# Kernel tuning notes

Hardware: AMD Instinct MI355X
Metric: run time of the kernel (lower is better)

Reference implementation:

```python
import jax, jax.numpy as jnp
import numpy as np
from jax import lax

TAU = 2.0        # LIFNode default tau, decay_input=True, v_reset=0.0
V_TH = 1.0       # default threshold
SG_ALPHA = 4.0   # surrogate.Sigmoid default alpha
EPS = 1e-5


@jax.custom_vjp
def spike_fn(v):
    return (v >= V_TH).astype(v.dtype)

def _spike_fwd(v):
    return spike_fn(v), v

def _spike_bwd(v, g):
    sg = jax.nn.sigmoid(SG_ALPHA * (v - V_TH))
    return (g * SG_ALPHA * sg * (1.0 - sg),)

spike_fn.defvjp(_spike_fwd, _spike_bwd)


def lif(x_seq):
    """Multi-step LIF: x_seq [T, ...] -> spikes [T, ...]. Hard reset to 0."""
    def step(v, x):
        v = v + (x - v) / TAU          # decay_input integration, v_reset=0
        s = spike_fn(v)
        v = v * (1.0 - s)              # hard reset
        return v, s
    v0 = jnp.zeros_like(x_seq[0])
    _, s_seq = lax.scan(step, v0, x_seq)
    return s_seq


def conv3x3(x, w):
    # x [N,C,H,W], w [O,I,3,3], padding=1, no bias
    return lax.conv_general_dilated(x, w, (1, 1), ((1, 1), (1, 1)),
                                    dimension_numbers=('NCHW', 'OIHW', 'NCHW'))


def tdbn(x, gamma, beta):
    # ThresholdDependentBatchNorm2d: BN over merged (T*B, H, W) per channel
    m = x.mean(axis=(0, 2, 3), keepdims=True)
    v = x.var(axis=(0, 2, 3), keepdims=True)
    return (x - m) * lax.rsqrt(v + EPS) * gamma[None, :, None, None] + beta[None, :, None, None]


def maxpool2(x):
    return lax.reduce_window(x, -jnp.inf, lax.max, (1, 1, 2, 2), (1, 1, 2, 2), 'VALID')


def setup_inputs() -> dict:
    key = jax.random.key(0)
    ks = jax.random.split(key, 5)
    T, B, H, W = 16, 32, 32, 400
    x = jax.random.normal(ks[0], (T, B, 1, H, W), dtype=jnp.float32)
    w1 = jax.random.normal(ks[1], (6, 1, 3, 3), dtype=jnp.float32) * (1.0 / 3.0)
    w2 = jax.random.normal(ks[2], (6, 6, 3, 3), dtype=jnp.float32) * (1.0 / jnp.sqrt(54.0))
    w3 = jax.random.normal(ks[3], (6, 6, 3, 3), dtype=jnp.float32) * (1.0 / jnp.sqrt(54.0))
    kf = jax.random.split(ks[4], 2)
    fw1 = jax.random.normal(kf[0], (100, 1200), dtype=jnp.float32) * (1.0 / jnp.sqrt(1200.0))
    fw2 = jax.random.normal(kf[1], (2, 100), dtype=jnp.float32) * (1.0 / 10.0)
    ones6 = jnp.ones((6,), jnp.float32)
    zeros6 = jnp.zeros((6,), jnp.float32)
    return {"x": x, "w1": w1, "g1": ones6, "b1": zeros6,
            "w2": w2, "g2": ones6, "b2": zeros6,
            "w3": w3, "g3": ones6, "b3": zeros6,
            "fw1": fw1, "fw2": fw2}


def _forward(x, w1, g1, b1, w2, g2, b2, w3, g3, b3, fw1, fw2):
    T, B = x.shape[0], x.shape[1]

    def block(s_seq, w, g, b):
        # conv + tdBN + LIF + maxpool over [T,B,C,H,W]
        TB = s_seq.reshape((T * B,) + s_seq.shape[2:])
        y = tdbn(conv3x3(TB, w), g, b)
        y = y.reshape((T, B) + y.shape[1:])
        s = lif(y)
        p = maxpool2(s.reshape((T * B,) + s.shape[2:]))
        return p.reshape((T, B) + p.shape[1:])

    h = block(x, w1, g1, b1)
    h = block(h, w2, g2, b2)
    h = block(h, w3, g3, b3)          # [T, B, 6, 4, 50]

    h = h.reshape(T, B, -1)            # flatten (C,H,W) -> 1200
    h = lif(jnp.einsum('tbf,of->tbo', h, fw1))   # [T, B, 100]
    out = lif(jnp.einsum('tbf,of->tbo', h, fw2)) # [T, B, 2]
    return out


def reference(x, w1, g1, b1, w2, g2, b2, w3, g3, b3, fw1, fw2):
    return _forward(x, w1, g1, b1, w2, g2, b2, w3, g3, b3, fw1, fw2)
```

## Files before the change

kernel.cpp:

```cpp
#include <hip/hip_runtime.h>


namespace {

constexpr int T = 16, B = 32;
constexpr int H1 = 32, W1 = 400, P1H = 16, P1W = 200;
constexpr int H2 = 16, W2 = 200, P2H = 8,  P2W = 100;
constexpr int H3 = 8,  W3 = 100, P3H = 4,  P3W = 50;

constexpr int NWG_S1 = T * B * (H1 / 32) * (W1 / 100);
constexpr int NWG_F1 = B * (P1H / 4) * (P1W / 10);
constexpr int NWG_F2 = B * (P2H / 4) * (P2W / 5);

constexpr size_t OFF_PART1  = 0;
constexpr size_t OFF_PARTF1 = OFF_PART1 + (size_t)NWG_S1 * 12 * 8;
constexpr size_t OFF_PARTF2 = OFF_PARTF1 + (size_t)6400 * 12 * 8;
constexpr size_t OFF_STATS  = OFF_PARTF2 + (size_t)2560 * 12 * 8;
constexpr size_t OFF_POOL1  = 1310720;
constexpr size_t OFF_POOL2  = OFF_POOL1 + (size_t)T * B * 6 * P1H * P1W * 4;
constexpr size_t OFF_POOL3  = OFF_POOL2 + (size_t)T * B * 6 * P2H * P2W * 4;
constexpr size_t OFF_U1     = OFF_POOL3 + (size_t)T * B * 6 * P3H * P3W * 4;

}

#define LDS_PHASE_BARRIER()                                   \
  do {                                                        \
    asm volatile("s_waitcnt lgkmcnt(0)" ::: "memory");        \
    __builtin_amdgcn_s_barrier();                             \
    __builtin_amdgcn_sched_barrier(0);                        \
  } while (0)

__device__ __forceinline__ float lif_step(float& v, float y) {
  v = v + (y - v) * 0.5f;
  float sp = (v >= 1.0f) ? 1.0f : 0.0f;
  v = (sp > 0.0f) ? 0.0f : v;
  return sp;
}

__device__ __forceinline__ void reduce12(double* s, double* q, double* partials) {
  __shared__ double lds[4][12];
  int lane = threadIdx.x & 63, wid = threadIdx.x >> 6;
#pragma unroll
  for (int k = 0; k < 12; k++) {
    double v = (k < 6) ? s[k] : q[k - 6];
#pragma unroll
    for (int off = 32; off >= 1; off >>= 1) v += __shfl_down(v, off, 64);
    if (lane == 0) lds[wid][k] = v;
  }
  __syncthreads();
  if (threadIdx.x < 12) {
    partials[(size_t)blockIdx.x * 12 + threadIdx.x] =
        lds[0][threadIdx.x] + lds[1][threadIdx.x] + lds[2][threadIdx.x] + lds[3][threadIdx.x];
  }
}

__device__ __forceinline__ void reduce12_sel(int oidx, double s_acc, double q_acc,
                                             double* partials) {
  __shared__ double lds[4][12];
  int lane = threadIdx.x & 63, wid = threadIdx.x >> 6;
#pragma unroll
  for (int k = 0; k < 12; k++) {
    double v = (k == oidx) ? s_acc : ((k == oidx + 6) ? q_acc : 0.0);
#pragma unroll
    for (int off = 32; off >= 1; off >>= 1) v += __shfl_down(v, off, 64);
    if (lane == 0) lds[wid][k] = v;
  }
  __syncthreads();
  if (threadIdx.x < 12) {
    partials[(size_t)blockIdx.x * 12 + threadIdx.x] =
        lds[0][threadIdx.x] + lds[1][threadIdx.x] + lds[2][threadIdx.x] + lds[3][threadIdx.x];
  }
}

template <int NC, int H, int W, int TH, int TW>
__global__ void conv_stats_lds(const float* __restrict__ in, const float* __restrict__ wt,
                               double* __restrict__ partials) {
  constexpr int IH = TH + 2, IW = TW + 2;
  constexpr int IWP = (IW & 1) ? IW : IW + 1;
  constexpr int NW = NC * 54;
  constexpr int NTH = H / TH, NTW = W / TW;
  constexpr int NT = NTH * NTW;
  __shared__ float wsm[NW];
  __shared__ float tile[NC][IH][IWP];

  int tid = threadIdx.x;
  for (int k = tid; k < NW; k += blockDim.x) wsm[k] = wt[k];

  int wg = blockIdx.x;
  int tb = wg / NT;
  int ti = wg % NT;
  int ty = ti / NTW, tx = ti % NTW;
  int h0 = ty * TH - 1, w0 = tx * TW - 1;
  const float* xb = in + (size_t)tb * NC * H * W;

  for (int k = tid; k < NC * IH * IW; k += blockDim.x) {
    int i = k / (IH * IW);
    int r = k % (IH * IW);
    int rr = r / IW, cc = r % IW;
    int hh = h0 + rr, ww = w0 + cc;
    tile[i][rr][cc] = (hh >= 0 && hh < H && ww >= 0 && ww < W) ? xb[i * H * W + hh * W + ww] : 0.0f;
  }
  __syncthreads();

  double s[6] = {0, 0, 0, 0, 0, 0}, q[6] = {0, 0, 0, 0, 0, 0};
  for (int pos = tid; pos < TH * TW; pos += blockDim.x) {
    int ly = pos / TW, lx = pos % TW;
    float acc[6] = {0, 0, 0, 0, 0, 0};
#pragma unroll
    for (int i = 0; i < NC; i++) {
      float p[9];
#pragma unroll
      for (int ky = 0; ky < 3; ky++)
#pragma unroll
        for (int kx = 0; kx < 3; kx++) p[ky * 3 + kx] = tile[i][ly + ky][lx + kx];
#pragma unroll
      for (int o = 0; o < 6; o++) {
        float a = acc[o];
#pragma unroll
        for (int k2 = 0; k2 < 9; k2++) a = fmaf(p[k2], wsm[(o * NC + i) * 9 + k2], a);
        acc[o] = a;
      }
    }
#pragma unroll
    for (int o = 0; o < 6; o++) {
      s[o] += (double)acc[o];
      q[o] += (double)acc[o] * (double)acc[o];
    }
  }
  reduce12(s, q, partials);
}

__global__ void finalize_stats(const double* __restrict__ partials, int nb, double n,
                               const float* __restrict__ gamma,
                               float* __restrict__ mean_out, float* __restrict__ sg_out) {
  __shared__ double red0[256];
  __shared__ double red1[256];
  int ch = blockIdx.x;
  int tid = threadIdx.x;
  double a0 = 0.0, a1 = 0.0;
  for (int b = tid; b < nb; b += 256) {
    a0 += partials[(size_t)b * 12 + ch];
    a1 += partials[(size_t)b * 12 + ch + 6];
  }
  red0[tid] = a0;
  red1[tid] = a1;
  __syncthreads();
#pragma unroll
  for (int off = 128; off >= 1; off >>= 1) {
    if (tid < off) {
      red0[tid] += red0[tid + off];
      red1[tid] += red1[tid + off];
    }
    __syncthreads();
  }
  if (tid == 0) {
    double mean = red0[0] / n;
    double var = red1[0] / n - mean * mean;
    double invstd = 1.0 / sqrt(var + 1e-5);
    mean_out[ch] = (float)mean;
    sg_out[ch] = (float)(invstd * (double)gamma[ch]);
  }
}

__global__ void fuse1_stats(const float* __restrict__ x, const float* __restrict__ w1g,
                            const float* __restrict__ w2g,
                            const float* __restrict__ mean1, const float* __restrict__ sg1,
                            const float* __restrict__ beta1,
                            float* __restrict__ pool1, double* __restrict__ partials2) {
  __shared__ float wsm1[54];
  __shared__ float wsm2[324];
  __shared__ float til[2][14][13];
  __shared__ float phl[432];
  __shared__ float pr[40][7][7];

  int tid = threadIdx.x;
  for (int k = tid; k < 54; k += 256) wsm1[k] = w1g[k];
  for (int k = tid; k < 324; k += 256) wsm2[k] = w2g[k];

  int wg = blockIdx.x;
  int b = wg / 80;
  int rem = wg % 80;
  int oy = rem / 20, ox = rem % 20;
  int iy0 = 8 * oy - 3, ix0 = 20 * ox - 3;

  bool s_in[2];
  int s_off[2], s_lofs[2];
#pragma unroll
  for (int j = 0; j < 2; j++) {
    int k = tid + 256 * j;
    bool valid = k < 364;
    int srr = k / 26, scc = k % 26;
    int shh = iy0 + srr, sww = ix0 + scc;
    s_in[j] = valid && shh >= 0 && shh < H1 && sww >= 0 && sww < W1;
    s_off[j] = shh * W1 + sww;
    s_lofs[j] = valid ? ((scc & 1) * 182 + srr * 13 + (scc >> 1)) : -1;
  }
  float* tilf = &til[0][0][0];

  int hch[2], hhy[2], hhx[2], hpy[2], hpx[2];
  bool hact[2], hval[2], hown[2];
  float m_[2], sc_[2], be_[2];
  float wv[2][9];
#pragma unroll
  for (int sl = 0; sl < 2; sl++) {
    int pos = tid + 256 * sl;
    hact[sl] = pos < 432;
    int p2 = hact[sl] ? pos : 0;
    int ch = p2 / 72;
    int r = p2 % 72;
    int hy = r / 12, hx = r % 12;
    hch[sl] = ch; hhy[sl] = hy; hhx[sl] = hx;
    int py = 4 * oy - 1 + hy, px = 10 * ox - 1 + hx;
    hpy[sl] = py; hpx[sl] = px;
    hval[sl] = hact[sl] && py >= 0 && py < P1H && px >= 0 && px < P1W;
    hown[sl] = hact[sl] && hy >= 1 && hy <= 4 && hx >= 1 && hx <= 10;
#pragma unroll
    for (int k = 0; k < 9; k++) wv[sl][k] = w1g[ch * 9 + k];
    m_[sl] = mean1[ch]; sc_[sl] = sg1[ch]; be_[sl] = beta1[ch];
  }

  int oidx = (tid < 240) ? (tid / 40) : -1;
  int pos40 = tid % 40;
  int psy = pos40 / 10, psx = pos40 % 10;

  float v[2][4];
#pragma unroll
  for (int sl = 0; sl < 2; sl++)
#pragma unroll
    for (int k = 0; k < 4; k++) v[sl][k] = 0.0f;
  double s_acc = 0.0, q_acc = 0.0;

  float rs[2] = {0.0f, 0.0f};
#pragma unroll
  for (int j = 0; j < 2; j++)
    if (s_in[j]) rs[j] = x[(size_t)(0 * B + b) * (H1 * W1) + s_off[j]];

  for (int t = 0; t < T; t++) {
    __syncthreads();
#pragma unroll
    for (int j = 0; j < 2; j++)
      if (s_lofs[j] >= 0) tilf[s_lofs[j]] = rs[j];
    if (t + 1 < T) {
#pragma unroll
      for (int j = 0; j < 2; j++)
        if (s_in[j]) rs[j] = x[(size_t)((t + 1) * B + b) * (H1 * W1) + s_off[j]];
    }
    LDS_PHASE_BARRIER();
#pragma unroll
    for (int sl = 0; sl < 2; sl++) {
      if (hact[sl]) {
        float smax = 0.0f;
        if (hval[sl]) {
          int ry = 2 * hhy[sl], hx = hhx[sl];
          float p[16];
#pragma unroll
          for (int r = 0; r < 4; r++) {
            p[r * 4 + 0] = til[0][ry + r][hx];
            p[r * 4 + 1] = til[1][ry + r][hx];
            p[r * 4 + 2] = til[0][ry + r][hx + 1];
            p[r * 4 + 3] = til[1][ry + r][hx + 1];
          }
#pragma unroll
          for (int dy = 0; dy < 2; dy++) {
#pragma unroll
            for (int dx = 0; dx < 2; dx++) {
              float acc = 0.0f;
#pragma unroll
              for (int ky = 0; ky < 3; ky++)
#pragma unroll
                for (int kx = 0; kx < 3; kx++)
                  acc = fmaf(p[(dy + ky) * 4 + dx + kx], wv[sl][ky * 3 + kx], acc);
              float y = (acc - m_[sl]) * sc_[sl] + be_[sl];
              float sp = lif_step(v[sl][dy * 2 + dx], y);
              smax = fmaxf(smax, sp);
            }
          }
        }
        phl[tid + 256 * sl] = smax;
        if (hown[sl])
          pool1[((size_t)(t * B + b) * 6 + hch[sl]) * (P1H * P1W) + hpy[sl] * P1W + hpx[sl]] = smax;
      }
    }
    LDS_PHASE_BARRIER();
    if (oidx >= 0) {
      int i2 = oidx;
      float pt[9];
#pragma unroll
      for (int ky = 0; ky < 3; ky++)
#pragma unroll
        for (int kx = 0; kx < 3; kx++)
          pt[ky * 3 + kx] = phl[i2 * 72 + (psy + ky) * 12 + (psx + kx)];
      float p6[6];
#pragma unroll
      for (int o = 0; o < 6; o++) {
        float a = 0.0f;
#pragma unroll
        for (int k2 = 0; k2 < 9; k2++) a = fmaf(pt[k2], wsm2[(o * 6 + i2) * 9 + k2], a);
        p6[o] = a;
      }
#pragma unroll
      for (int o = 0; o < 6; o++) pr[pos40][i2][o] = p6[o];
    }
    LDS_PHASE_BARRIER();
    if (oidx >= 0) {
      double acc = 0.0;
#pragma unroll
      for (int ic = 0; ic < 6; ic++) acc += (double)pr[pos40][ic][oidx];
      s_acc += acc;
      q_acc += acc * acc;
    }
  }
  __syncthreads();
  reduce12_sel(oidx, s_acc, q_acc, partials2);
}

__global__ void fuse2_stats(const float* __restrict__ in, const float* __restrict__ w2g,
                            const float* __restrict__ w3g,
                            const float* __restrict__ mean2, const float* __restrict__ sg2,
                            const float* __restrict__ beta2,
                            float* __restrict__ pool2, double* __restrict__ partials3) {
  __shared__ float wsm2[324];
  __shared__ float wsm3[324];
  __shared__ float til[2][6][14][9];
  __shared__ float phl[6][6][7];
  __shared__ float pr[20][6][7];

  int tid = threadIdx.x;
  for (int k = tid; k < 324; k += 256) { wsm2[k] = w2g[k]; wsm3[k] = w3g[k]; }

  int wg = blockIdx.x;
  int b = wg / 40;
  int rem = wg % 40;
  int oy = rem / 20, ox = rem % 20;
  int iy0 = 8 * oy - 3, ix0 = 10 * ox - 3;
  constexpr int HW = H2 * W2;

  bool s_in[6];
  int s_off[6], s_lofs[6];
#pragma unroll
  for (int j = 0; j < 6; j++) {
    int k = tid + 256 * j;
    bool valid = k < 1344;
    int i = k / 224;
    int r2 = k % 224;
    int rr = r2 / 16, cc = r2 % 16;
    int hh = iy0 + rr, ww = ix0 + cc;
    s_in[j] = valid && hh >= 0 && hh < H2 && ww >= 0 && ww < W2;
    s_off[j] = i * HW + hh * W2 + ww;
    s_lofs[j] = valid ? ((cc & 1) * 756 + i * 126 + rr * 9 + (cc >> 1)) : -1;
  }
  float* tilf = &til[0][0][0][0];

  bool active = tid < 252;
  int ch = 0, hy = 0, hx = 0, py = 0, px = 0;
  bool pvalid = false, own = false;
  if (active) {
    ch = tid / 42;
    int r = tid % 42;
    hy = r / 7; hx = r % 7;
    py = 4 * oy - 1 + hy; px = 5 * ox - 1 + hx;
    pvalid = (py >= 0 && py < P2H && px >= 0 && px < P2W);
    own = (hy >= 1 && hy <= 4 && hx >= 1 && hx <= 5);
  }
  float m = active ? mean2[ch] : 0.0f;
  float sc = active ? sg2[ch] : 0.0f;
  float be = active ? beta2[ch] : 0.0f;

  int oidx = (tid < 120) ? (tid / 20) : -1;
  int pos = tid % 20;
  int psy = pos / 5, psx = pos % 5;

  float v[4] = {0.0f, 0.0f, 0.0f, 0.0f};
  double s_acc = 0.0, q_acc = 0.0;

  float rs[6] = {0.0f, 0.0f, 0.0f, 0.0f, 0.0f, 0.0f};
  {
    const float* xb = in + (size_t)(0 * B + b) * 6 * HW;
#pragma unroll
    for (int j = 0; j < 6; j++)
      if (s_in[j]) rs[j] = xb[s_off[j]];
  }

  for (int t = 0; t < T; t++) {
    __syncthreads();
#pragma unroll
    for (int j = 0; j < 6; j++)
      if (s_lofs[j] >= 0) tilf[s_lofs[j]] = rs[j];
    if (t + 1 < T) {
      const float* xb = in + (size_t)((t + 1) * B + b) * 6 * HW;
#pragma unroll
      for (int j = 0; j < 6; j++)
        if (s_in[j]) rs[j] = xb[s_off[j]];
    }
    LDS_PHASE_BARRIER();
    if (active) {
      float smax = 0.0f;
      if (pvalid) {
        int ry = 2 * hy;
        float acc4[4] = {0.0f, 0.0f, 0.0f, 0.0f};
#pragma unroll
        for (int i = 0; i < 6; i++) {
          float p[16];
#pragma unroll
          for (int r = 0; r < 4; r++) {
            p[r * 4 + 0] = til[0][i][ry + r][hx];
            p[r * 4 + 1] = til[1][i][ry + r][hx];
            p[r * 4 + 2] = til[0][i][ry + r][hx + 1];
            p[r * 4 + 3] = til[1][i][ry + r][hx + 1];
          }
          const float* wo = &wsm2[(ch * 6 + i) * 9];
#pragma unroll
          for (int dy = 0; dy < 2; dy++)
#pragma unroll
            for (int dx = 0; dx < 2; dx++) {
              float a = acc4[dy * 2 + dx];
#pragma unroll
              for (int ky = 0; ky < 3; ky++)
#pragma unroll
                for (int kx = 0; kx < 3; kx++)
                  a = fmaf(p[(dy + ky) * 4 + dx + kx], wo[ky * 3 + kx], a);
              acc4[dy * 2 + dx] = a;
            }
        }
#pragma unroll
        for (int p4 = 0; p4 < 4; p4++) {
          float y = (acc4[p4] - m) * sc + be;
          float sp = lif_step(v[p4], y);
          smax = fmaxf(smax, sp);
        }
      }
      phl[ch][hy][hx] = smax;
      if (own)
        pool2[((size_t)(t * B + b) * 6 + ch) * (P2H * P2W) + py * P2W + px] = smax;
    }
    LDS_PHASE_BARRIER();
    if (oidx >= 0) {
      float pt[9];
#pragma unroll
      for (int ky = 0; ky < 3; ky++)
#pragma unroll
        for (int kx = 0; kx < 3; kx++)
          pt[ky * 3 + kx] = phl[oidx][psy + ky][psx + kx];
      float p6[6];
#pragma unroll
      for (int o = 0; o < 6; o++) {
        float a = 0.0f;
#pragma unroll
        for (int k2 = 0; k2 < 9; k2++) a = fmaf(pt[k2], wsm3[(o * 6 + oidx) * 9 + k2], a);
        p6[o] = a;
      }
#pragma unroll
      for (int o = 0; o < 6; o++) pr[pos][oidx][o] = p6[o];
    }
    LDS_PHASE_BARRIER();
    if (oidx >= 0) {
      double acc = 0.0;
#pragma unroll
      for (int ic = 0; ic < 6; ic++) acc += (double)pr[pos][ic][oidx];
      s_acc += acc;
      q_acc += acc * acc;
    }
  }
  __syncthreads();
  reduce12_sel(oidx, s_acc, q_acc, partials3);
}

template <int H, int W, int PH, int PW, int TH, int TW>
__global__ void block6_fuse_lds(const float* __restrict__ in, const float* __restrict__ wt,
                                const float* __restrict__ mean, const float* __restrict__ sg,
                                const float* __restrict__ beta, float* __restrict__ out) {
  constexpr int NTH = PH / TH, NTW = PW / TW;
  constexpr int IH = 2 * TH + 2, IW = 2 * TW + 2;
  constexpr int EW = IW / 2;
  constexpr int TILE_N = IH * IW;
  constexpr int NACT = 6 * TH * TW;
  constexpr int HW = H * W;
  __shared__ float wsm[324];
  __shared__ float til_e[6][IH][EW];
  __shared__ float til_o[6][IH][EW];

  for (int k = threadIdx.x; k < 324; k += blockDim.x) wsm[k] = wt[k];

  int wg = blockIdx.x;
  int b = wg / (NTH * NTW);
  int tid2 = wg % (NTH * NTW);
  int ty = tid2 / NTW, tx = tid2 % NTW;
  int h_in0 = 2 * (ty * TH) - 1, w_in0 = 2 * (tx * TW) - 1;

  int tid = threadIdx.x;
  int o = 0, lph = 0, lpw = 0;
  if (tid < NACT) {
    o = tid / (TH * TW);
    int r = tid % (TH * TW);
    lph = r / TW; lpw = r % TW;
  }
  float m = mean[o], s = sg[o], be = beta[o];
  float v[4] = {0.0f, 0.0f, 0.0f, 0.0f};

  for (int t = 0; t < T; t++) {
    __syncthreads();
    const float* xb = in + (size_t)(t * B + b) * 6 * HW;
    for (int k = tid; k < 6 * TILE_N; k += blockDim.x) {
      int i = k / TILE_N;
      int r2 = k % TILE_N;
      int rr = r2 / IW, cc = r2 % IW;
      int hh = h_in0 + rr, ww = w_in0 + cc;
      float val = (hh >= 0 && hh < H && ww >= 0 && ww < W) ? xb[i * HW + hh * W + ww] : 0.0f;
      if (cc & 1) til_o[i][rr][cc >> 1] = val;
      else        til_e[i][rr][cc >> 1] = val;
    }
    __syncthreads();
    if (tid < NACT) {
      int ry = 2 * lph;
      float acc[4] = {0.0f, 0.0f, 0.0f, 0.0f};
#pragma unroll
      for (int i = 0; i < 6; i++) {
        float p[16];
#pragma unroll
        for (int r = 0; r < 4; r++) {
          p[r * 4 + 0] = til_e[i][ry + r][lpw];
          p[r * 4 + 1] = til_o[i][ry + r][lpw];
          p[r * 4 + 2] = til_e[i][ry + r][lpw + 1];
          p[r * 4 + 3] = til_o[i][ry + r][lpw + 1];
        }
        const float* wo = &wsm[(o * 6 + i) * 9];
#pragma unroll
        for (int dy = 0; dy < 2; dy++)
#pragma unroll
          for (int dx = 0; dx < 2; dx++) {
            float a = acc[dy * 2 + dx];
#pragma unroll
            for (int ky = 0; ky < 3; ky++)
#pragma unroll
              for (int kx = 0; kx < 3; kx++)
                a = fmaf(p[(dy + ky) * 4 + dx + kx], wo[ky * 3 + kx], a);
            acc[dy * 2 + dx] = a;
          }
      }
      float smax = 0.0f;
#pragma unroll
      for (int p4 = 0; p4 < 4; p4++) {
        float y = (acc[p4] - m) * s + be;
        float sp = lif_step(v[p4], y);
        smax = fmaxf(smax, sp);
      }
      out[((size_t)(t * B + b) * 6 + o) * (PH * PW) + (ty * TH + lph) * PW + (tx * TW + lpw)] = smax;
    }
  }
}

__global__ void fc1_mm(const float* __restrict__ p3, const float* __restrict__ fw1,
                       float* __restrict__ u1) {
  int idx = blockIdx.x * blockDim.x + threadIdx.x;
  if (idx >= T * B * 100) return;
  int o = idx % 100;
  int tb = idx / 100;
  const float4* x4 = (const float4*)(p3 + (size_t)tb * 1200);
  const float4* w4 = (const float4*)(fw1 + (size_t)o * 1200);
  float acc = 0.0f;
#pragma unroll 4
  for (int k = 0; k < 300; k++) {
    float4 a = x4[k], w = w4[k];
    acc = fmaf(a.x, w.x, acc);
    acc = fmaf(a.y, w.y, acc);
    acc = fmaf(a.z, w.z, acc);
    acc = fmaf(a.w, w.w, acc);
  }
  u1[idx] = acc;
}

__global__ void fc_tail(const float* __restrict__ u1, const float* __restrict__ fw2,
                        float* __restrict__ outp) {
  __shared__ float s1[100];
  __shared__ float w2s[200];
  int b = blockIdx.x;
  int tid = threadIdx.x;
  for (int k = tid; k < 200; k += 128) w2s[k] = fw2[k];
  float v1 = 0.0f, v2 = 0.0f;
  __syncthreads();
  for (int t = 0; t < T; t++) {
    if (tid < 100) {
      float sp = lif_step(v1, u1[(size_t)(t * B + b) * 100 + tid]);
      s1[tid] = sp;
    }
    __syncthreads();
    if (tid < 2) {
      const float* wr = &w2s[tid * 100];
      float acc = 0.0f;
#pragma unroll
      for (int k = 0; k < 100; k++) acc = fmaf(s1[k], wr[k], acc);
      float sp = lif_step(v2, acc);
      outp[(size_t)(t * B + b) * 2 + tid] = sp;
    }
    __syncthreads();
  }
}

extern "C" void kernel_launch(void* const* d_in, const int* in_sizes, int n_in,
                              void* d_out, int out_size, void* d_ws, size_t ws_size,
                              hipStream_t stream) {
  const float* x   = (const float*)d_in[0];
  const float* w1  = (const float*)d_in[1];
  const float* g1  = (const float*)d_in[2];
  const float* b1  = (const float*)d_in[3];
  const float* w2  = (const float*)d_in[4];
  const float* g2  = (const float*)d_in[5];
  const float* b2  = (const float*)d_in[6];
  const float* w3  = (const float*)d_in[7];
  const float* g3  = (const float*)d_in[8];
  const float* b3  = (const float*)d_in[9];
  const float* fw1 = (const float*)d_in[10];
  const float* fw2 = (const float*)d_in[11];
  float* out = (float*)d_out;

  char* ws = (char*)d_ws;
  double* part1  = (double*)(ws + OFF_PART1);
  double* partf1 = (double*)(ws + OFF_PARTF1);
  double* partf2 = (double*)(ws + OFF_PARTF2);
  float* mean1 = (float*)(ws + OFF_STATS + 0);
  float* sg1   = (float*)(ws + OFF_STATS + 32);
  float* mean2 = (float*)(ws + OFF_STATS + 64);
  float* sg2   = (float*)(ws + OFF_STATS + 96);
  float* mean3 = (float*)(ws + OFF_STATS + 128);
  float* sg3   = (float*)(ws + OFF_STATS + 160);
  float* pool1 = (float*)(ws + OFF_POOL1);
  float* pool2 = (float*)(ws + OFF_POOL2);
  float* pool3 = (float*)(ws + OFF_POOL3);
  float* u1    = (float*)(ws + OFF_U1);

  conv_stats_lds<1, H1, W1, 32, 100><<<NWG_S1, 256, 0, stream>>>(x, w1, part1);
  finalize_stats<<<6, 256, 0, stream>>>(part1, NWG_S1, (double)T * B * H1 * W1, g1, mean1, sg1);
  fuse1_stats<<<NWG_F1, 256, 0, stream>>>(x, w1, w2, mean1, sg1, b1, pool1, partf1);
  finalize_stats<<<6, 256, 0, stream>>>(partf1, NWG_F1, (double)T * B * H2 * W2, g2, mean2, sg2);
  fuse2_stats<<<NWG_F2, 256, 0, stream>>>(pool1, w2, w3, mean2, sg2, b2, pool2, partf2);
  finalize_stats<<<6, 256, 0, stream>>>(partf2, NWG_F2, (double)T * B * H3 * W3, g3, mean3, sg3);
  {
    int nwg = B * (P3H / 2) * (P3W / 5);
    block6_fuse_lds<H3, W3, P3H, P3W, 2, 5><<<nwg, 64, 0, stream>>>(pool2, w3, mean3, sg3, b3, pool3);
  }
  {
    int n = T * B * 100;
    fc1_mm<<<(n + 255) / 256, 256, 0, stream>>>(pool3, fw1, u1);
  }
  fc_tail<<<B, 128, 0, stream>>>(u1, fw2, out);
}
```

Before: 368.7 us.

## Restructure FC1 as per-row workgroup with wave reductions; parallelize FC2 dot

```diff
diff --git a/kernel.cpp b/kernel.cpp
--- a/kernel.cpp
+++ b/kernel.cpp
@@ -551,22 +551,21 @@
 
 __global__ void fc1_mm(const float* __restrict__ p3, const float* __restrict__ fw1,
                        float* __restrict__ u1) {
-  int idx = blockIdx.x * blockDim.x + threadIdx.x;
-  if (idx >= T * B * 100) return;
-  int o = idx % 100;
-  int tb = idx / 100;
-  const float4* x4 = (const float4*)(p3 + (size_t)tb * 1200);
-  const float4* w4 = (const float4*)(fw1 + (size_t)o * 1200);
-  float acc = 0.0f;
-#pragma unroll 4
-  for (int k = 0; k < 300; k++) {
-    float4 a = x4[k], w = w4[k];
-    acc = fmaf(a.x, w.x, acc);
-    acc = fmaf(a.y, w.y, acc);
-    acc = fmaf(a.z, w.z, acc);
-    acc = fmaf(a.w, w.w, acc);
-  }
-  u1[idx] = acc;
+  __shared__ float xp[1200];
+  int tb = blockIdx.x;
+  int tid = threadIdx.x;
+  const float* xr = p3 + (size_t)tb * 1200;
+  for (int k = tid; k < 1200; k += 256) xp[k] = xr[k];
+  __syncthreads();
+  int wave = tid >> 6, lane = tid & 63;
+  for (int o = wave; o < 100; o += 4) {
+    const float* wr = fw1 + (size_t)o * 1200;
+    float acc = 0.0f;
+    for (int k = lane; k < 1200; k += 64) acc = fmaf(xp[k], wr[k], acc);
+#pragma unroll
+    for (int off = 32; off >= 1; off >>= 1) acc += __shfl_down(acc, off, 64);
+    if (lane == 0) u1[(size_t)tb * 100 + o] = acc;
+  }
 }
 
 __global__ void fc_tail(const float* __restrict__ u1, const float* __restrict__ fw2,
@@ -576,6 +575,7 @@
   int b = blockIdx.x;
   int tid = threadIdx.x;
   for (int k = tid; k < 200; k += 128) w2s[k] = fw2[k];
+  int wave = tid >> 6, lane = tid & 63;
   float v1 = 0.0f, v2 = 0.0f;
   __syncthreads();
   for (int t = 0; t < T; t++) {
@@ -584,13 +584,16 @@
       s1[tid] = sp;
     }
     __syncthreads();
-    if (tid < 2) {
-      const float* wr = &w2s[tid * 100];
-      float acc = 0.0f;
-#pragma unroll
-      for (int k = 0; k < 100; k++) acc = fmaf(s1[k], wr[k], acc);
-      float sp = lif_step(v2, acc);
-      outp[(size_t)(t * B + b) * 2 + tid] = sp;
+    {
+      const float* wr = &w2s[wave * 100];
+      float acc = s1[lane] * wr[lane];
+      if (lane < 36) acc = fmaf(s1[lane + 64], wr[lane + 64], acc);
+#pragma unroll
+      for (int off = 32; off >= 1; off >>= 1) acc += __shfl_down(acc, off, 64);
+      if (lane == 0) {
+        float sp = lif_step(v2, acc);
+        outp[(size_t)(t * B + b) * 2 + wave] = sp;
+      }
     }
     __syncthreads();
   }
@@ -638,9 +641,6 @@
     int nwg = B * (P3H / 2) * (P3W / 5);
     block6_fuse_lds<H3, W3, P3H, P3W, 2, 5><<<nwg, 64, 0, stream>>>(pool2, w3, mean3, sg3, b3, pool3);
   }
-  {
-    int n = T * B * 100;
-    fc1_mm<<<(n + 255) / 256, 256, 0, stream>>>(pool3, fw1, u1);
-  }
+  fc1_mm<<<T * B, 256, 0, stream>>>(pool3, fw1, u1);
   fc_tail<<<B, 128, 0, stream>>>(u1, fw2, out);
 }
```

New measurement: 466.5 us. +26.5%, slower.
